# Kernel tuning notes

Hardware: AMD Instinct MI355X
Metric: run time of the kernel (lower is better)

The kernel has to match this reference:

```python
import jax, jax.numpy as jnp
import numpy as np

NEG_INF = -1000000000.0
NEG_SLOPE = 0.01  # torch leaky_relu default

N, IN_F, OUT_F = 8192, 256, 128


def setup_inputs() -> dict:
    key = jax.random.key(0)
    k1, k2, k3, k4 = jax.random.split(key, 4)
    x = jax.random.normal(k1, (N, IN_F), dtype=jnp.float32)
    adj = jax.random.randint(k2, (N, N), 0, 2, dtype=jnp.int32)
    W = jax.random.normal(k3, (IN_F, OUT_F), dtype=jnp.float32) * (1.0 / np.sqrt(IN_F))
    a = jax.random.normal(k4, (2 * OUT_F,), dtype=jnp.float32) * (1.0 / np.sqrt(2 * OUT_F))
    return {"x": x, "adj": adj, "W": W, "a": a}


def reference(x, adj, W, a):
    # h = W(x): [N, out]
    h = x @ W
    out_f = h.shape[1]
    # a([h_i || h_j]) == h_i @ a1 + h_j @ a2 -- same math, no [N,N,2F] tensor
    a1, a2 = a[:out_f], a[out_f:]
    f1 = h @ a1  # [N]
    f2 = h @ a2  # [N]
    e = jax.nn.leaky_relu(f1[:, None] + f2[None, :], negative_slope=NEG_SLOPE)  # [N, N]
    masked = jnp.where(adj > 0, e, NEG_INF)
    attention = jax.nn.softmax(masked, axis=1)
    return attention @ h, attention
```

## Files before the change

### kernel.cpp

```cpp
#include <hip/hip_runtime.h>
#include <hip/hip_bf16.h>

constexpr int NROW = 8192;
constexpr int INF  = 256;
constexpr int OUTF = 128;
constexpr int KSPLIT = 8;
constexpr int KCHUNK = NROW / KSPLIT;
constexpr int NIT    = KCHUNK / 64;
#define LOG2E 1.4426950408889634f

typedef __bf16 bf16x8 __attribute__((ext_vector_type(8)));
typedef float  f32x4  __attribute__((ext_vector_type(4)));
typedef int    i32x4  __attribute__((ext_vector_type(4)));
typedef unsigned long long u64;

__global__ __launch_bounds__(256) void k1(const float* __restrict__ x,
                                          const float* __restrict__ W,
                                          const float* __restrict__ a,
                                          __bf16* __restrict__ ht,
                                          float* __restrict__ f1,
                                          float* __restrict__ f2) {
  __shared__ float xs[32][INF];
  __shared__ float hs[32][OUTF];
  const int t  = threadIdx.x;
  const int i0 = blockIdx.x * 32;

  const f32x4* xsrc = reinterpret_cast<const f32x4*>(x + (size_t)i0 * INF);
  f32x4* xdst = reinterpret_cast<f32x4*>(&xs[0][0]);
  #pragma unroll
  for (int u = 0; u < (32 * INF / 4) / 256; ++u)
    xdst[u * 256 + t] = xsrc[u * 256 + t];
  __syncthreads();

  const int c  = t & 127;
  const int rg = t >> 7;
  float acc[16];
  #pragma unroll
  for (int r = 0; r < 16; ++r) acc[r] = 0.f;
  for (int k = 0; k < INF; ++k) {
    float wv = W[k * OUTF + c];
    #pragma unroll
    for (int r = 0; r < 16; ++r) acc[r] += xs[rg * 16 + r][k] * wv;
  }
  #pragma unroll
  for (int r = 0; r < 16; ++r) hs[rg * 16 + r][c] = acc[r];
  __syncthreads();

  const int wv = t >> 6, lane = t & 63;
  for (int r = wv; r < 32; r += 4) {
    float h0 = hs[r][lane * 2], h1 = hs[r][lane * 2 + 1];
    float s1 = h0 * a[lane * 2] + h1 * a[lane * 2 + 1];
    float s2 = h0 * a[OUTF + lane * 2] + h1 * a[OUTF + lane * 2 + 1];
    #pragma unroll
    for (int off = 32; off; off >>= 1) {
      s1 += __shfl_down(s1, off);
      s2 += __shfl_down(s2, off);
    }
    if (lane == 0) { f1[i0 + r] = s1 * LOG2E; f2[i0 + r] = s2 * LOG2E; }
  }

  const int col = t >> 1, seg = t & 1;
  bf16x8 v0, v1;
  #pragma unroll
  for (int r = 0; r < 8; ++r) v0[r] = (__bf16)hs[seg * 16 + r][col];
  #pragma unroll
  for (int r = 0; r < 8; ++r) v1[r] = (__bf16)hs[seg * 16 + 8 + r][col];
  __bf16* hdst = ht + (size_t)col * NROW + i0 + seg * 16;
  *reinterpret_cast<bf16x8*>(hdst)     = v0;
  *reinterpret_cast<bf16x8*>(hdst + 8) = v1;
}

__global__ __launch_bounds__(256) void katt2(const int* __restrict__ adj,
                                             const float* __restrict__ f1,
                                             const float* __restrict__ f2,
                                             u64* __restrict__ mask,
                                             float* __restrict__ s,
                                             float* __restrict__ att) {
  const int i = blockIdx.x;
  const int t = threadIdx.x;
  const int lane = t & 63, wv = t >> 6;
  const float f1i = f1[i];
  const i32x4* arow = reinterpret_cast<const i32x4*>(adj + (size_t)i * NROW);
  const f32x4* f2v  = reinterpret_cast<const f32x4*>(f2);
  u64* mrow = mask + (size_t)i * 128;

  unsigned mynibs = 0;
  float acc = 0.f;
  f32x4 fv[8];
  #pragma unroll
  for (int it = 0; it < 8; ++it) {
    i32x4 av = __builtin_nontemporal_load(arow + it * 256 + t);
    fv[it] = f2v[it * 256 + t];
    unsigned nib = (av[0] > 0) | ((av[1] > 0) << 1) | ((av[2] > 0) << 2) |
                   ((av[3] > 0) << 3);
    mynibs |= nib << (it * 4);
    #pragma unroll
    for (int b = 0; b < 4; ++b) {
      float e = f1i + fv[it][b];
      e = e > 0.f ? e : 0.01f * e;
      acc += ((nib >> b) & 1u) ? __builtin_exp2f(e) : 0.f;
    }
  }

  #pragma unroll
  for (int it = 0; it < 8; ++it) {
    u64 m = (u64)((mynibs >> (it * 4)) & 0xFu) << (4 * (lane & 15));
    #pragma unroll
    for (int d = 1; d < 16; d <<= 1) m |= __shfl_xor(m, d);
    if ((lane & 15) == 0) mrow[it * 16 + (t >> 4)] = m;
  }
  #pragma unroll
  for (int off = 32; off; off >>= 1) acc += __shfl_down(acc, off);
  __shared__ float red[4];
  if (lane == 0) red[wv] = acc;
  __syncthreads();
  const float srow = red[0] + red[1] + red[2] + red[3];
  if (t == 0) s[i] = srow;
  const float inv_s = 1.0f / srow;

  f32x4* adst = reinterpret_cast<f32x4*>(att + (size_t)i * NROW);
  #pragma unroll
  for (int it = 0; it < 8; ++it) {
    const unsigned nib = (mynibs >> (it * 4)) & 0xFu;
    f32x4 o;
    #pragma unroll
    for (int b = 0; b < 4; ++b) {
      float e = f1i + fv[it][b];
      e = e > 0.f ? e : 0.01f * e;
      o[b] = ((nib >> b) & 1u) ? __builtin_exp2f(e) * inv_s : 0.f;
    }
    adst[it * 256 + t] = o;
  }
}

__global__ __launch_bounds__(256, 4) void kpv(const __bf16* __restrict__ ht,
                                              const float* __restrict__ f1,
                                              const float* __restrict__ f2,
                                              const float* __restrict__ sum,
                                              const u64* __restrict__ mask,
                                              float* __restrict__ out0) {
  __shared__ float f2s[KCHUNK];
  __shared__ u64 ms[64][17];
  const int mb = blockIdx.x / KSPLIT;
  const int ks = blockIdx.x % KSPLIT;
  const int t    = threadIdx.x;
  const int w    = t >> 6;
  const int wr   = w >> 1;
  const int wc   = w & 1;
  const int lane = t & 63;
  const int lr = lane & 15;
  const int lc = lane >> 4;
  const int row0 = mb * 64;
  const int j0 = ks * KCHUNK;

  {
    reinterpret_cast<f32x4*>(f2s)[t] =
        reinterpret_cast<const f32x4*>(f2 + j0)[t];
    const int r = t >> 2, q = (t & 3) * 4;
    const u64* msrc = mask + (size_t)(row0 + r) * 128 + (j0 >> 6) + q;
    ms[r][q]     = msrc[0];
    ms[r][q + 1] = msrc[1];
    ms[r][q + 2] = msrc[2];
    ms[r][q + 3] = msrc[3];
  }
  __syncthreads();

  const float f1r0 = f1[row0 + wr * 32 + lr];
  const float f1r1 = f1[row0 + wr * 32 + 16 + lr];
  const __bf16* hbase =
      ht + (size_t)(wc * 64 + lr) * NROW + j0 + lc * 8;

  f32x4 acc[2][4];
  #pragma unroll
  for (int rt = 0; rt < 2; ++rt)
    #pragma unroll
    for (int n = 0; n < 4; ++n) acc[rt][n] = (f32x4){0.f, 0.f, 0.f, 0.f};

  for (int it = 0; it < NIT; ++it) {
    const int kk = it * 64;

    bf16x8 b[4][2];
    #pragma unroll
    for (int n = 0; n < 4; ++n) {
      const __bf16* hb = hbase + (size_t)(n * 16) * NROW + kk;
      b[n][0] = *reinterpret_cast<const bf16x8*>(hb);
      b[n][1] = *reinterpret_cast<const bf16x8*>(hb + 32);
    }

    const u64 mw0 = ms[wr * 32 + lr][it];
    const u64 mw1 = ms[wr * 32 + 16 + lr][it];
    bf16x8 afrag[2][2];
    #pragma unroll
    for (int h = 0; h < 2; ++h) {
      const int base = kk + h * 32 + lc * 8;
      const f32x4 fa = *reinterpret_cast<const f32x4*>(&f2s[base]);
      const f32x4 fb = *reinterpret_cast<const f32x4*>(&f2s[base + 4]);
      const unsigned bits0 = (unsigned)(mw0 >> (h * 32 + lc * 8)) & 0xFFu;
      const unsigned bits1 = (unsigned)(mw1 >> (h * 32 + lc * 8)) & 0xFFu;
      #pragma unroll
      for (int i2 = 0; i2 < 8; ++i2) {
        const float fval = (i2 < 4) ? fa[i2] : fb[i2 - 4];
        float e0 = f1r0 + fval;
        e0 = e0 > 0.f ? e0 : 0.01f * e0;
        afrag[0][h][i2] =
            (__bf16)(((bits0 >> i2) & 1u) ? __builtin_exp2f(e0) : 0.f);
        float e1 = f1r1 + fval;
        e1 = e1 > 0.f ? e1 : 0.01f * e1;
        afrag[1][h][i2] =
            (__bf16)(((bits1 >> i2) & 1u) ? __builtin_exp2f(e1) : 0.f);
      }
    }

    #pragma unroll
    for (int rt = 0; rt < 2; ++rt)
      #pragma unroll
      for (int n = 0; n < 4; ++n) {
        acc[rt][n] = __builtin_amdgcn_mfma_f32_16x16x32_bf16(
            afrag[rt][0], b[n][0], acc[rt][n], 0, 0, 0);
        acc[rt][n] = __builtin_amdgcn_mfma_f32_16x16x32_bf16(
            afrag[rt][1], b[n][1], acc[rt][n], 0, 0, 0);
      }
  }

  #pragma unroll
  for (int rt = 0; rt < 2; ++rt) {
    float inv_sD[4];
    #pragma unroll
    for (int i2 = 0; i2 < 4; ++i2)
      inv_sD[i2] = 1.0f / sum[row0 + wr * 32 + rt * 16 + lc * 4 + i2];
    #pragma unroll
    for (int n = 0; n < 4; ++n) {
      #pragma unroll
      for (int i2 = 0; i2 < 4; ++i2) {
        atomicAdd(&out0[(size_t)(row0 + wr * 32 + rt * 16 + lc * 4 + i2) * OUTF +
                        wc * 64 + n * 16 + lr],
                  acc[rt][n][i2] * inv_sD[i2]);
      }
    }
  }
}

extern "C" void kernel_launch(void* const* d_in, const int* in_sizes, int n_in,
                              void* d_out, int out_size, void* d_ws, size_t ws_size,
                              hipStream_t stream) {
  const float* x   = (const float*)d_in[0];
  const int*   adj = (const int*)d_in[1];
  const float* W   = (const float*)d_in[2];
  const float* a   = (const float*)d_in[3];

  float* out0 = (float*)d_out;
  float* att  = (float*)d_out + (size_t)NROW * OUTF;

  char* ws = (char*)d_ws;
  __bf16* ht = (__bf16*)ws;
  u64* mask = (u64*)(ws + (2 << 20));
  float* f1 = (float*)(ws + (10 << 20));
  float* f2 = (float*)(ws + (10 << 20) + 32 * 1024);
  float* s  = (float*)(ws + (10 << 20) + 64 * 1024);

  hipMemsetAsync(out0, 0, (size_t)NROW * OUTF * sizeof(float), stream);
  k1<<<NROW / 32, 256, 0, stream>>>(x, W, a, ht, f1, f2);
  katt2<<<NROW, 256, 0, stream>>>(adj, f1, f2, mask, s, att);
  kpv<<<(NROW / 64) * KSPLIT, 256, 0, stream>>>(ht, f1, f2, s, mask, out0);
}
```

Baseline: 201.5 us.

## Stage ht tiles through double-buffered LDS with register prefetch in kpv

Replaces the per-wave direct global loads of ht B-fragments in the PV kernel with a cooperative copy of each 128x64 bf16 tile into padded shared memory, double-buffered. The next tile is prefetched into registers while exp/MFMA work runs, then written to the alternate buffer ahead of a barrier. This aims to hide global load latency and let the two row-waves share each B tile, at the cost of about 37KB more LDS, a block barrier per iteration, and lower declared occupancy (launch bounds 4 to 3).

```diff
diff --git a/kernel.cpp b/kernel.cpp
--- a/kernel.cpp
+++ b/kernel.cpp
@@ -133,12 +133,13 @@
   }
 }
 
-__global__ __launch_bounds__(256, 4) void kpv(const __bf16* __restrict__ ht,
+__global__ __launch_bounds__(256, 3) void kpv(const __bf16* __restrict__ ht,
                                               const float* __restrict__ f1,
                                               const float* __restrict__ f2,
                                               const float* __restrict__ sum,
                                               const u64* __restrict__ mask,
                                               float* __restrict__ out0) {
+  __shared__ __bf16 bs[2][128][72];
   __shared__ float f2s[KCHUNK];
   __shared__ u64 ms[64][17];
   const int mb = blockIdx.x / KSPLIT;
@@ -163,12 +164,22 @@
     ms[r][q + 2] = msrc[2];
     ms[r][q + 3] = msrc[3];
   }
+  const int sr = t >> 1, sc = (t & 1) * 32;
+  const __bf16* sgsrc = ht + (size_t)sr * NROW + j0 + sc;
+  {
+    bf16x8 st0 = *reinterpret_cast<const bf16x8*>(sgsrc);
+    bf16x8 st1 = *reinterpret_cast<const bf16x8*>(sgsrc + 8);
+    bf16x8 st2 = *reinterpret_cast<const bf16x8*>(sgsrc + 16);
+    bf16x8 st3 = *reinterpret_cast<const bf16x8*>(sgsrc + 24);
+    *reinterpret_cast<bf16x8*>(&bs[0][sr][sc])      = st0;
+    *reinterpret_cast<bf16x8*>(&bs[0][sr][sc + 8])  = st1;
+    *reinterpret_cast<bf16x8*>(&bs[0][sr][sc + 16]) = st2;
+    *reinterpret_cast<bf16x8*>(&bs[0][sr][sc + 24]) = st3;
+  }
   __syncthreads();
 
   const float f1r0 = f1[row0 + wr * 32 + lr];
   const float f1r1 = f1[row0 + wr * 32 + 16 + lr];
-  const __bf16* hbase =
-      ht + (size_t)(wc * 64 + lr) * NROW + j0 + lc * 8;
 
   f32x4 acc[2][4];
   #pragma unroll
@@ -177,14 +188,17 @@
     for (int n = 0; n < 4; ++n) acc[rt][n] = (f32x4){0.f, 0.f, 0.f, 0.f};
 
   for (int it = 0; it < NIT; ++it) {
+    const int cur = it & 1;
+    const bool more = (it + 1) < NIT;
     const int kk = it * 64;
 
-    bf16x8 b[4][2];
-    #pragma unroll
-    for (int n = 0; n < 4; ++n) {
-      const __bf16* hb = hbase + (size_t)(n * 16) * NROW + kk;
-      b[n][0] = *reinterpret_cast<const bf16x8*>(hb);
-      b[n][1] = *reinterpret_cast<const bf16x8*>(hb + 32);
+    bf16x8 st0, st1, st2, st3;
+    if (more) {
+      const __bf16* sg = sgsrc + (it + 1) * 64;
+      st0 = *reinterpret_cast<const bf16x8*>(sg);
+      st1 = *reinterpret_cast<const bf16x8*>(sg + 8);
+      st2 = *reinterpret_cast<const bf16x8*>(sg + 16);
+      st3 = *reinterpret_cast<const bf16x8*>(sg + 24);
     }
 
     const u64 mw0 = ms[wr * 32 + lr][it];
@@ -212,14 +226,27 @@
     }
 
     #pragma unroll
-    for (int rt = 0; rt < 2; ++rt)
+    for (int n = 0; n < 4; ++n) {
+      bf16x8 b0 = *reinterpret_cast<const bf16x8*>(
+          &bs[cur][wc * 64 + n * 16 + lr][lc * 8]);
+      bf16x8 b1 = *reinterpret_cast<const bf16x8*>(
+          &bs[cur][wc * 64 + n * 16 + lr][lc * 8 + 32]);
       #pragma unroll
-      for (int n = 0; n < 4; ++n) {
+      for (int rt = 0; rt < 2; ++rt) {
         acc[rt][n] = __builtin_amdgcn_mfma_f32_16x16x32_bf16(
-            afrag[rt][0], b[n][0], acc[rt][n], 0, 0, 0);
+            afrag[rt][0], b0, acc[rt][n], 0, 0, 0);
         acc[rt][n] = __builtin_amdgcn_mfma_f32_16x16x32_bf16(
-            afrag[rt][1], b[n][1], acc[rt][n], 0, 0, 0);
+            afrag[rt][1], b1, acc[rt][n], 0, 0, 0);
       }
+    }
+
+    if (more) {
+      *reinterpret_cast<bf16x8*>(&bs[cur ^ 1][sr][sc])      = st0;
+      *reinterpret_cast<bf16x8*>(&bs[cur ^ 1][sr][sc + 8])  = st1;
+      *reinterpret_cast<bf16x8*>(&bs[cur ^ 1][sr][sc + 16]) = st2;
+      *reinterpret_cast<bf16x8*>(&bs[cur ^ 1][sr][sc + 24]) = st3;
+      __syncthreads();
+    }
   }
 
   #pragma unroll
```

Measured after the change: 204.2 us. Within noise of the previous version (+1.4%).
